# Performance work log

Hardware: AMD Instinct MI355X
Metric: run time of the kernel (lower is better)

## Reference

```python
import jax, jax.numpy as jnp
import numpy as np

EPS = 1e-5

def _conv1x1(x, w, b):
    # x: [B,C,H,W], w: [O,C], b: [O]  (1x1 conv == channel matmul)
    return jnp.einsum('bchw,oc->bohw', x, w) + b[None, :, None, None]

def _bn_relu(y, gamma, beta, mean, var):
    inv = gamma / jnp.sqrt(var + EPS)
    return jax.nn.relu(y * inv[None, :, None, None] + (beta - mean * inv)[None, :, None, None])

def setup_inputs() -> dict:
    key = jax.random.key(0)
    ks = jax.random.split(key, 8)
    B, C, H, W = 8, 2048, 48, 48
    mid = C // 4  # k = 4 -> mid_ch = 512
    s_in = (2.0 / C) ** 0.5   # kaiming-like scale for 1x1 convs from C channels
    s_mid = (2.0 / mid) ** 0.5
    return {
        'x': jax.random.normal(ks[0], (B, C, H, W), jnp.float32),
        'f_w': jax.random.normal(ks[1], (mid, C), jnp.float32) * s_in,
        'f_b': jnp.zeros((mid,), jnp.float32),
        'f_gamma': jnp.ones((mid,), jnp.float32),
        'f_beta': jnp.zeros((mid,), jnp.float32),
        'f_mean': jnp.zeros((mid,), jnp.float32),
        'f_var': jnp.ones((mid,), jnp.float32),
        'g_w': jax.random.normal(ks[2], (mid, C), jnp.float32) * s_in,
        'g_b': jnp.zeros((mid,), jnp.float32),
        'g_gamma': jnp.ones((mid,), jnp.float32),
        'g_beta': jnp.zeros((mid,), jnp.float32),
        'g_mean': jnp.zeros((mid,), jnp.float32),
        'g_var': jnp.ones((mid,), jnp.float32),
        'h_w': jax.random.normal(ks[3], (mid, C), jnp.float32) * s_in,
        'h_b': jnp.zeros((mid,), jnp.float32),
        'v_w': jax.random.normal(ks[4], (C, mid), jnp.float32) * s_mid,
        'v_b': jnp.zeros((C,), jnp.float32),
    }

def reference(x, f_w, f_b, f_gamma, f_beta, f_mean, f_var,
              g_w, g_b, g_gamma, g_beta, g_mean, g_var,
              h_w, h_b, v_w, v_b):
    B, C, H, W = x.shape
    mid = f_w.shape[0]
    N = H * W
    f_x = _bn_relu(_conv1x1(x, f_w, f_b), f_gamma, f_beta, f_mean, f_var).reshape(B, mid, N)
    g_x = _bn_relu(_conv1x1(x, g_w, g_b), g_gamma, g_beta, g_mean, g_var).reshape(B, mid, N)
    h_x = _conv1x1(x, h_w, h_b).reshape(B, mid, N)
    # z = f_x^T @ g_x : [B, N, N]
    scores = jnp.einsum('bcn,bcm->bnm', f_x, g_x) * (mid ** -0.5)
    attn = jax.nn.softmax(scores, axis=-1)
    # z = attn @ h_x^T : [B, N, mid] -> [B, mid, H, W]
    z = jnp.einsum('bnm,bcm->bcn', attn, h_x).reshape(B, mid, H, W)
    z = jnp.einsum('bchw,oc->bohw', z, v_w) + v_b[None, :, None, None]
    return (z + x, attn)
```

## Files before the change

kernel.cpp:

```cpp
#include <hip/hip_runtime.h>
#include <math.h>

typedef unsigned short u16;
typedef unsigned short u16x4 __attribute__((ext_vector_type(4)));
typedef unsigned short u16x8 __attribute__((ext_vector_type(8)));
typedef __bf16 bf16x8 __attribute__((ext_vector_type(8)));
typedef float f32x4 __attribute__((ext_vector_type(4)));

typedef __attribute__((address_space(1))) const unsigned int gu32;
typedef __attribute__((address_space(3))) unsigned int su32;

#define B_ 8
#define C_ 2048
#define MID_ 512
#define N_ 2304

#define BAR() do { asm volatile("" ::: "memory"); __builtin_amdgcn_s_barrier(); asm volatile("" ::: "memory"); } while (0)

#define QMFMA(AV, BV, MO, NO)                                                             \
  { _Pragma("unroll") for (int mfi = 0; mfi < 4; ++mfi) {                                 \
      _Pragma("unroll") for (int nfi = 0; nfi < 2; ++nfi) {                               \
        acc[MO + mfi][NO + nfi] = __builtin_amdgcn_mfma_f32_16x16x32_bf16(                \
            AV[0][mfi], BV[0][nfi], acc[MO + mfi][NO + nfi], 0, 0, 0);                    \
        acc[MO + mfi][NO + nfi] = __builtin_amdgcn_mfma_f32_16x16x32_bf16(                \
            AV[1][mfi], BV[1][nfi], acc[MO + mfi][NO + nfi], 0, 0, 0); } } }

static __device__ __forceinline__ u16 f2bf(float f) {
  union { float f; unsigned u; } c; c.f = f;
  unsigned u = c.u;
  u += 0x7fffu + ((u >> 16) & 1u);
  return (u16)(u >> 16);
}
static __device__ __forceinline__ float bf2f(u16 x) {
  union { unsigned u; float f; } c; c.u = ((unsigned)x) << 16; return c.f;
}

__global__ __launch_bounds__(256) void prep_all_k(
    const float* __restrict__ fw, const float* __restrict__ gw,
    const float* __restrict__ hw, const float* __restrict__ vw,
    const float* fb, const float* fg, const float* fbe, const float* fm, const float* fv,
    const float* gb, const float* gg, const float* gbe, const float* gm, const float* gv,
    const float* hb,
    u16* __restrict__ wall, u16* __restrict__ vwb,
    float* __restrict__ scale, float* __restrict__ bias) {
  const int gid = blockIdx.x * 256 + threadIdx.x;
  if (gid < 393216) {
    int e = gid * 8; int r = e >> 11;
    const float* s = (r < 512) ? (fw + e) : (r < 1024) ? (gw + e - (512 << 11)) : (hw + e - (1024 << 11));
    float4 v0 = *(const float4*)s, v1 = *(const float4*)(s + 4);
    u16x8 w;
    w[0]=f2bf(v0.x); w[1]=f2bf(v0.y); w[2]=f2bf(v0.z); w[3]=f2bf(v0.w);
    w[4]=f2bf(v1.x); w[5]=f2bf(v1.y); w[6]=f2bf(v1.z); w[7]=f2bf(v1.w);
    *(u16x8*)&wall[e] = w;
  } else if (gid < 524288) {
    int e = (gid - 393216) * 8;
    float4 v0 = *(const float4*)(vw + e), v1 = *(const float4*)(vw + e + 4);
    u16x8 w;
    w[0]=f2bf(v0.x); w[1]=f2bf(v0.y); w[2]=f2bf(v0.z); w[3]=f2bf(v0.w);
    w[4]=f2bf(v1.x); w[5]=f2bf(v1.y); w[6]=f2bf(v1.z); w[7]=f2bf(v1.w);
    *(u16x8*)&vwb[e] = w;
  }
  if (gid < 1536) {
    const float FS = 0.044194173824159216f;
    int i = gid;
    if (i < 512) {
      float inv = fg[i] / sqrtf(fv[i] + 1e-5f);
      scale[i] = inv * FS; bias[i] = (fb[i] * inv + fbe[i] - fm[i] * inv) * FS;
    } else if (i < 1024) {
      int j = i - 512;
      float inv = gg[j] / sqrtf(gv[j] + 1e-5f);
      scale[i] = inv; bias[i] = gb[j] * inv + gbe[j] - gm[j] * inv;
    } else {
      scale[i] = 1.0f; bias[i] = hb[i - 1024];
    }
  }
}

__global__ __launch_bounds__(256) void transpose_x_k(const float* __restrict__ x, u16* __restrict__ xT) {
  __shared__ float tile[64][68];
  const int b = blockIdx.z;
  const int n0 = blockIdx.x * 64, c0 = blockIdx.y * 64;
  const float* xb = x + (size_t)b * C_ * N_;
  u16* xTb = xT + (size_t)b * N_ * C_;
  const int r = threadIdx.x >> 2, q = threadIdx.x & 3;
  #pragma unroll
  for (int j = 0; j < 4; ++j) {
    float4 v = *(const float4*)&xb[(size_t)(c0 + r) * N_ + n0 + (q + 4 * j) * 4];
    *(float4*)&tile[r][(q + 4 * j) * 4] = v;
  }
  __syncthreads();
  #pragma unroll
  for (int g = 0; g < 2; ++g) {
    const int cl = (q * 2 + g) * 8;
    u16x8 w;
    #pragma unroll
    for (int e = 0; e < 8; ++e) w[e] = f2bf(tile[cl + e][r]);
    *(u16x8*)&xTb[(size_t)(n0 + r) * C_ + c0 + cl] = w;
  }
}

__global__ __launch_bounds__(256) void transpose_h_k(const u16* __restrict__ fghT, u16* __restrict__ hx) {
  __shared__ u16 tile[64][72];
  const int b = blockIdx.z;
  const int n0 = blockIdx.x * 64, c0 = blockIdx.y * 64;
  const u16* src = fghT + (size_t)b * N_ * 1536;
  u16* dst = hx + (size_t)b * MID_ * N_;
  const int r = threadIdx.x >> 2, q = threadIdx.x & 3;
  #pragma unroll
  for (int g = 0; g < 2; ++g) {
    const int cl = q * 16 + g * 8;
    *(u16x8*)&tile[r][cl] = *(const u16x8*)&src[(size_t)(n0 + r) * 1536 + 1024 + c0 + cl];
  }
  __syncthreads();
  #pragma unroll
  for (int g = 0; g < 2; ++g) {
    const int cl = q * 16 + g * 8;
    u16x8 w;
    #pragma unroll
    for (int e = 0; e < 8; ++e) w[e] = tile[cl + e][r];
    *(u16x8*)&dst[(size_t)(c0 + r) * N_ + n0 + cl] = w;
  }
}

#define EP_FG 0
#define EP_SCALE16 1
#define EP_FINAL 2

template<int EPI, int SWZ, int GX, int GY>
__global__ __launch_bounds__(512, 2) void gemm5_kernel(
    const u16* __restrict__ Ag, int lda, long long sA,
    const u16* __restrict__ Bg, int ldb, long long sB,
    void* __restrict__ Cg, int ldc, long long sC, int K,
    const float* __restrict__ ep_scale, const float* __restrict__ ep_bias,
    const float* __restrict__ ep_x, long long sX)
{
  extern __shared__ __align__(16) u16 smem[];
  u16* As = smem;
  u16* Bs = smem + 2 * 256 * 64;

  int tx, ty, tz;
  {
    const int L = blockIdx.x;
    const int xcd = L & 7, r = L >> 3;
    if constexpr (SWZ == 0) {
      const int i = r % GX, j = (r / GX) * 8 + xcd;
      tx = i; ty = j % GY; tz = j / GY;
    } else if constexpr (SWZ == 1) {
      const int i = r % GY, j = (r / GY) * 8 + xcd;
      ty = i; tx = j % GX; tz = j / GX;
    } else {
      const int i = r % 9, jg = (r / 9) * 8 + xcd;
      const int bx = jg % (GX / 3), rem = jg / (GX / 3);
      const int by = rem % (GY / 3); tz = rem / (GY / 3);
      tx = bx * 3 + i % 3; ty = by * 3 + i / 3;
    }
  }

  const int tid = threadIdx.x;
  const int lane = tid & 63;
  const int wv = tid >> 6;
  const int b = tz;
  const int m0 = ty * 256;
  const int n0 = tx * 256;
  const int wm = (wv >> 2) * 128;
  const int wn = (wv & 3) * 64;
  const int lr = lane & 15, lg = lane >> 4;

  const u16* Ab = Ag + (size_t)b * sA;
  const u16* Bb = Bg + (size_t)b * sB;
  const int nk = K >> 6;

  const int srow = lane >> 3;
  const int sksw = ((lane & 7) ^ srow) * 8;
  const int rdsw0 = ((0 + lg) ^ (lr & 7)) * 8;
  const int rdsw1 = ((4 + lg) ^ (lr & 7)) * 8;

  f32x4 acc[8][4];
  #pragma unroll
  for (int i = 0; i < 8; ++i)
    #pragma unroll
    for (int j = 0; j < 4; ++j)
      acc[i][j] = f32x4{0.f, 0.f, 0.f, 0.f};

  auto STAGE_A = [&](int p2, int t) {
    #pragma unroll
    for (int j = 0; j < 4; ++j) {
      const int rb = j * 64 + wv * 8;
      const u16* g = Ab + (size_t)(m0 + rb + srow) * lda + t * 64 + sksw;
      __builtin_amdgcn_global_load_lds((gu32*)g, (su32*)(As + p2 * 16384 + rb * 64), 16, 0, 0);
    }
  };
  auto STAGE_B = [&](int p2, int t) {
    #pragma unroll
    for (int j = 0; j < 4; ++j) {
      const int rb = j * 64 + wv * 8;
      const u16* g = Bb + (size_t)(n0 + rb + srow) * ldb + t * 64 + sksw;
      __builtin_amdgcn_global_load_lds((gu32*)g, (su32*)(Bs + p2 * 16384 + rb * 64), 16, 0, 0);
    }
  };

  STAGE_A(0, 0); STAGE_B(0, 0);
  if (nk > 1) { STAGE_A(1, 1); STAGE_B(1, 1); }

  for (int kt = 0; kt < nk; ++kt) {
    const int p = kt & 1;
    if (kt + 1 < nk) asm volatile("s_waitcnt vmcnt(8)" ::: "memory");
    else             asm volatile("s_waitcnt vmcnt(0)" ::: "memory");
    BAR();

    const u16* Asl = As + p * 16384;
    const u16* Bsl = Bs + p * 16384;
    const bool st = (kt + 2) < nk;
    const int ps = (kt + 2) & 1;

    bf16x8 aV[2][4], bLo[2][2], bHi[2][2];

    #pragma unroll
    for (int ks = 0; ks < 2; ++ks) {
      const int ro = ks ? rdsw1 : rdsw0;
      #pragma unroll
      for (int i = 0; i < 4; ++i)
        aV[ks][i] = *(const bf16x8*)(Asl + (wm + i * 16 + lr) * 64 + ro);
      #pragma unroll
      for (int i = 0; i < 2; ++i)
        bLo[ks][i] = *(const bf16x8*)(Bsl + (wn + i * 16 + lr) * 64 + ro);
    }
    BAR();
    __builtin_amdgcn_s_setprio(1);
    QMFMA(aV, bLo, 0, 0);
    __builtin_amdgcn_s_setprio(0);
    BAR();

    #pragma unroll
    for (int ks = 0; ks < 2; ++ks) {
      const int ro = ks ? rdsw1 : rdsw0;
      #pragma unroll
      for (int i = 0; i < 2; ++i)
        bHi[ks][i] = *(const bf16x8*)(Bsl + (wn + 32 + i * 16 + lr) * 64 + ro);
    }
    BAR();
    __builtin_amdgcn_s_setprio(1);
    QMFMA(aV, bHi, 0, 2);
    __builtin_amdgcn_s_setprio(0);
    BAR();

    #pragma unroll
    for (int ks = 0; ks < 2; ++ks) {
      const int ro = ks ? rdsw1 : rdsw0;
      #pragma unroll
      for (int i = 0; i < 4; ++i)
        aV[ks][i] = *(const bf16x8*)(Asl + (wm + 64 + i * 16 + lr) * 64 + ro);
    }
    if (st) STAGE_B(ps, kt + 2);
    BAR();
    __builtin_amdgcn_s_setprio(1);
    QMFMA(aV, bLo, 4, 0);
    __builtin_amdgcn_s_setprio(0);
    BAR();

    if (st) STAGE_A(ps, kt + 2);
    BAR();
    __builtin_amdgcn_s_setprio(1);
    QMFMA(aV, bHi, 4, 2);
    __builtin_amdgcn_s_setprio(0);
    BAR();
  }

  u16*   C16 = (u16*)Cg + (size_t)b * sC;
  float* C32 = (float*)Cg + (size_t)b * sC;
  const float* xb = (EPI == EP_FINAL) ? (ep_x + (size_t)b * sX) : nullptr;
  #pragma unroll
  for (int mf = 0; mf < 8; ++mf) {
    #pragma unroll
    for (int nf = 0; nf < 4; ++nf) {
      #pragma unroll
      for (int r = 0; r < 4; ++r) {
        int row = m0 + wm + mf * 16 + lg * 4 + r;
        int col = n0 + wn + nf * 16 + lr;
        float v = acc[mf][nf][r];
        if constexpr (EPI == EP_FG) {
          v = v * ep_scale[col] + ep_bias[col];
          if (col < 1024) v = fmaxf(v, 0.f);
          C16[(size_t)row * ldc + col] = f2bf(v);
        } else if constexpr (EPI == EP_SCALE16) {
          C16[(size_t)row * ldc + col] = f2bf(v);
        } else {
          v += ep_bias[row] + xb[(size_t)row * ldc + col];
          C32[(size_t)row * ldc + col] = v;
        }
      }
    }
  }
}

__global__ __launch_bounds__(256) void softmax_k(u16* __restrict__ SP, float* __restrict__ attn) {
  const int l = threadIdx.x & 63;
  const size_t row = (size_t)blockIdx.x * 4 + (threadIdx.x >> 6);
  u16* sp = SP + row * N_;
  float* ar = attn + row * N_;

  u16x8 s[4];
  #pragma unroll
  for (int j = 0; j < 4; ++j) s[j] = *(const u16x8*)&sp[j * 512 + l * 8];
  u16x4 st4 = *(const u16x4*)&sp[2048 + l * 4];

  float v[4][8], t[4];
  float mx = -3.0e38f;
  #pragma unroll
  for (int j = 0; j < 4; ++j)
    #pragma unroll
    for (int e = 0; e < 8; ++e) { v[j][e] = bf2f(s[j][e]); mx = fmaxf(mx, v[j][e]); }
  #pragma unroll
  for (int e = 0; e < 4; ++e) { t[e] = bf2f(st4[e]); mx = fmaxf(mx, t[e]); }
  #pragma unroll
  for (int o = 32; o; o >>= 1) mx = fmaxf(mx, __shfl_xor(mx, o));

  float sum = 0.f;
  #pragma unroll
  for (int j = 0; j < 4; ++j)
    #pragma unroll
    for (int e = 0; e < 8; ++e) { v[j][e] = __expf(v[j][e] - mx); sum += v[j][e]; }
  #pragma unroll
  for (int e = 0; e < 4; ++e) { t[e] = __expf(t[e] - mx); sum += t[e]; }
  #pragma unroll
  for (int o = 32; o; o >>= 1) sum += __shfl_xor(sum, o);
  const float inv = 1.0f / sum;

  #pragma unroll
  for (int j = 0; j < 4; ++j) {
    float4 lo = {v[j][0] * inv, v[j][1] * inv, v[j][2] * inv, v[j][3] * inv};
    float4 hi = {v[j][4] * inv, v[j][5] * inv, v[j][6] * inv, v[j][7] * inv};
    *(float4*)&ar[j * 512 + l * 8] = lo;
    *(float4*)&ar[j * 512 + l * 8 + 4] = hi;
    u16x8 p8;
    p8[0]=f2bf(lo.x); p8[1]=f2bf(lo.y); p8[2]=f2bf(lo.z); p8[3]=f2bf(lo.w);
    p8[4]=f2bf(hi.x); p8[5]=f2bf(hi.y); p8[6]=f2bf(hi.z); p8[7]=f2bf(hi.w);
    *(u16x8*)&sp[j * 512 + l * 8] = p8;
  }
  float4 tl = {t[0] * inv, t[1] * inv, t[2] * inv, t[3] * inv};
  *(float4*)&ar[2048 + l * 4] = tl;
  u16x4 p4; p4[0]=f2bf(tl.x); p4[1]=f2bf(tl.y); p4[2]=f2bf(tl.z); p4[3]=f2bf(tl.w);
  *(u16x4*)&sp[2048 + l * 4] = p4;
}

extern "C" void kernel_launch(void* const* d_in, const int* in_sizes, int n_in,
                              void* d_out, int out_size, void* d_ws, size_t ws_size,
                              hipStream_t stream) {
  const float* x    = (const float*)d_in[0];
  const float* f_w  = (const float*)d_in[1];
  const float* f_b  = (const float*)d_in[2];
  const float* f_ga = (const float*)d_in[3];
  const float* f_be = (const float*)d_in[4];
  const float* f_me = (const float*)d_in[5];
  const float* f_va = (const float*)d_in[6];
  const float* g_w  = (const float*)d_in[7];
  const float* g_b  = (const float*)d_in[8];
  const float* g_ga = (const float*)d_in[9];
  const float* g_be = (const float*)d_in[10];
  const float* g_me = (const float*)d_in[11];
  const float* g_va = (const float*)d_in[12];
  const float* h_w  = (const float*)d_in[13];
  const float* h_b  = (const float*)d_in[14];
  const float* v_w  = (const float*)d_in[15];
  const float* v_b  = (const float*)d_in[16];

  float* out0 = (float*)d_out;
  float* attn = out0 + (size_t)B_ * C_ * N_;

  char* p = (char*)d_ws;
  u16* xT   = (u16*)p; p += (size_t)B_ * N_ * C_ * 2;
  u16* fghT = (u16*)p; p += (size_t)B_ * N_ * 1536 * 2;
  u16* hx   = (u16*)p; p += (size_t)B_ * MID_ * N_ * 2;
  u16* ZT   = (u16*)p; p += (size_t)B_ * N_ * MID_ * 2;
  u16* Wall = (u16*)p; p += (size_t)1536 * C_ * 2;
  u16* vwb  = (u16*)p; p += (size_t)C_ * MID_ * 2;
  float* sc = (float*)p; p += 1536 * 4;
  float* bi = (float*)p; p += 1536 * 4;
  p = (char*)(((size_t)p + 255) & ~(size_t)255);
  u16* SP   = (u16*)p; p += (size_t)B_ * N_ * N_ * 2;

  hipFuncSetAttribute((const void*)gemm5_kernel<EP_FG, 0, 6, 9>,      hipFuncAttributeMaxDynamicSharedMemorySize, 131072);
  hipFuncSetAttribute((const void*)gemm5_kernel<EP_SCALE16, 2, 9, 9>, hipFuncAttributeMaxDynamicSharedMemorySize, 131072);
  hipFuncSetAttribute((const void*)gemm5_kernel<EP_SCALE16, 0, 2, 9>, hipFuncAttributeMaxDynamicSharedMemorySize, 131072);
  hipFuncSetAttribute((const void*)gemm5_kernel<EP_FINAL, 1, 9, 8>,   hipFuncAttributeMaxDynamicSharedMemorySize, 131072);

  prep_all_k<<<2048, 256, 0, stream>>>(f_w, g_w, h_w, v_w,
                                       f_b, f_ga, f_be, f_me, f_va,
                                       g_b, g_ga, g_be, g_me, g_va, h_b,
                                       Wall, vwb, sc, bi);
  transpose_x_k<<<dim3(N_ / 64, C_ / 64, B_), 256, 0, stream>>>(x, xT);

  gemm5_kernel<EP_FG, 0, 6, 9><<<dim3(6 * 9 * 8), 512, 131072, stream>>>(
      xT, C_, (long long)N_ * C_, Wall, C_, 0,
      fghT, 1536, (long long)N_ * 1536, C_, sc, bi, nullptr, 0);

  transpose_h_k<<<dim3(N_ / 64, MID_ / 64, B_), 256, 0, stream>>>(fghT, hx);

  gemm5_kernel<EP_SCALE16, 2, 9, 9><<<dim3(9 * 9 * 8), 512, 131072, stream>>>(
      fghT, 1536, (long long)N_ * 1536, fghT + 512, 1536, (long long)N_ * 1536,
      SP, N_, (long long)N_ * N_, MID_, nullptr, nullptr, nullptr, 0);

  softmax_k<<<(B_ * N_) / 4, 256, 0, stream>>>(SP, attn);

  gemm5_kernel<EP_SCALE16, 0, 2, 9><<<dim3(2 * 9 * 8), 512, 131072, stream>>>(
      SP, N_, (long long)N_ * N_, hx, N_, (long long)MID_ * N_,
      ZT, MID_, (long long)N_ * MID_, N_, nullptr, nullptr, nullptr, 0);

  gemm5_kernel<EP_FINAL, 1, 9, 8><<<dim3(9 * 8 * 8), 512, 131072, stream>>>(
      vwb, MID_, 0, ZT, MID_, (long long)N_ * MID_,
      out0, N_, (long long)C_ * N_, MID_, nullptr, v_b, x, (long long)C_ * N_);
}
```

Measured before the change: 504.3 us.

## Merge prep/transpose launches and stage bf16 GEMM epilogue through LDS

Merges the weight prep kernel into the x transpose kernel, and the h transpose into the softmax kernel, by splitting each launch's block range. This removes two kernel launches and lets the smaller jobs fill in around the larger ones. The bf16 GEMM epilogues now write each 16-row fragment into a free LDS buffer and read it back as 16-byte row segments, replacing scattered 2-byte global stores. The risk is that the reused LDS buffer could still be live for other waves, and the extra LDS round trip adds latency.

```diff
diff --git a/kernel.cpp b/kernel.cpp
--- a/kernel.cpp
+++ b/kernel.cpp
@@ -35,7 +35,8 @@
   union { unsigned u; float f; } c; c.u = ((unsigned)x) << 16; return c.f;
 }
 
-__global__ __launch_bounds__(256) void prep_all_k(
+__global__ __launch_bounds__(256) void txp_k(
+    const float* __restrict__ x, u16* __restrict__ xT,
     const float* __restrict__ fw, const float* __restrict__ gw,
     const float* __restrict__ hw, const float* __restrict__ vw,
     const float* fb, const float* fg, const float* fbe, const float* fm, const float* fv,
@@ -43,82 +44,59 @@
     const float* hb,
     u16* __restrict__ wall, u16* __restrict__ vwb,
     float* __restrict__ scale, float* __restrict__ bias) {
-  const int gid = blockIdx.x * 256 + threadIdx.x;
-  if (gid < 393216) {
-    int e = gid * 8; int r = e >> 11;
-    const float* s = (r < 512) ? (fw + e) : (r < 1024) ? (gw + e - (512 << 11)) : (hw + e - (1024 << 11));
-    float4 v0 = *(const float4*)s, v1 = *(const float4*)(s + 4);
-    u16x8 w;
-    w[0]=f2bf(v0.x); w[1]=f2bf(v0.y); w[2]=f2bf(v0.z); w[3]=f2bf(v0.w);
-    w[4]=f2bf(v1.x); w[5]=f2bf(v1.y); w[6]=f2bf(v1.z); w[7]=f2bf(v1.w);
-    *(u16x8*)&wall[e] = w;
-  } else if (gid < 524288) {
-    int e = (gid - 393216) * 8;
-    float4 v0 = *(const float4*)(vw + e), v1 = *(const float4*)(vw + e + 4);
-    u16x8 w;
-    w[0]=f2bf(v0.x); w[1]=f2bf(v0.y); w[2]=f2bf(v0.z); w[3]=f2bf(v0.w);
-    w[4]=f2bf(v1.x); w[5]=f2bf(v1.y); w[6]=f2bf(v1.z); w[7]=f2bf(v1.w);
-    *(u16x8*)&vwb[e] = w;
-  }
-  if (gid < 1536) {
-    const float FS = 0.044194173824159216f;
-    int i = gid;
-    if (i < 512) {
-      float inv = fg[i] / sqrtf(fv[i] + 1e-5f);
-      scale[i] = inv * FS; bias[i] = (fb[i] * inv + fbe[i] - fm[i] * inv) * FS;
-    } else if (i < 1024) {
-      int j = i - 512;
-      float inv = gg[j] / sqrtf(gv[j] + 1e-5f);
-      scale[i] = inv; bias[i] = gb[j] * inv + gbe[j] - gm[j] * inv;
-    } else {
-      scale[i] = 1.0f; bias[i] = hb[i - 1024];
-    }
-  }
-}
-
-__global__ __launch_bounds__(256) void transpose_x_k(const float* __restrict__ x, u16* __restrict__ xT) {
   __shared__ float tile[64][68];
-  const int b = blockIdx.z;
-  const int n0 = blockIdx.x * 64, c0 = blockIdx.y * 64;
-  const float* xb = x + (size_t)b * C_ * N_;
-  u16* xTb = xT + (size_t)b * N_ * C_;
-  const int r = threadIdx.x >> 2, q = threadIdx.x & 3;
-  #pragma unroll
-  for (int j = 0; j < 4; ++j) {
-    float4 v = *(const float4*)&xb[(size_t)(c0 + r) * N_ + n0 + (q + 4 * j) * 4];
-    *(float4*)&tile[r][(q + 4 * j) * 4] = v;
-  }
-  __syncthreads();
-  #pragma unroll
-  for (int g = 0; g < 2; ++g) {
-    const int cl = (q * 2 + g) * 8;
-    u16x8 w;
-    #pragma unroll
-    for (int e = 0; e < 8; ++e) w[e] = f2bf(tile[cl + e][r]);
-    *(u16x8*)&xTb[(size_t)(n0 + r) * C_ + c0 + cl] = w;
-  }
-}
-
-__global__ __launch_bounds__(256) void transpose_h_k(const u16* __restrict__ fghT, u16* __restrict__ hx) {
-  __shared__ u16 tile[64][72];
-  const int b = blockIdx.z;
-  const int n0 = blockIdx.x * 64, c0 = blockIdx.y * 64;
-  const u16* src = fghT + (size_t)b * N_ * 1536;
-  u16* dst = hx + (size_t)b * MID_ * N_;
-  const int r = threadIdx.x >> 2, q = threadIdx.x & 3;
-  #pragma unroll
-  for (int g = 0; g < 2; ++g) {
-    const int cl = q * 16 + g * 8;
-    *(u16x8*)&tile[r][cl] = *(const u16x8*)&src[(size_t)(n0 + r) * 1536 + 1024 + c0 + cl];
-  }
-  __syncthreads();
-  #pragma unroll
-  for (int g = 0; g < 2; ++g) {
-    const int cl = q * 16 + g * 8;
-    u16x8 w;
-    #pragma unroll
-    for (int e = 0; e < 8; ++e) w[e] = tile[cl + e][r];
-    *(u16x8*)&dst[(size_t)(c0 + r) * N_ + n0 + cl] = w;
+  const int bid = blockIdx.x;
+  if (bid < 9216) {
+    const int n0 = (bid % 36) * 64, c0 = ((bid / 36) % 32) * 64, b = bid / 1152;
+    const float* xb = x + (size_t)b * C_ * N_;
+    u16* xTb = xT + (size_t)b * N_ * C_;
+    const int r = threadIdx.x >> 2, q = threadIdx.x & 3;
+    #pragma unroll
+    for (int j = 0; j < 4; ++j) {
+      float4 v = *(const float4*)&xb[(size_t)(c0 + r) * N_ + n0 + (q + 4 * j) * 4];
+      *(float4*)&tile[r][(q + 4 * j) * 4] = v;
+    }
+    __syncthreads();
+    #pragma unroll
+    for (int g = 0; g < 2; ++g) {
+      const int cl = (q * 2 + g) * 8;
+      u16x8 w;
+      #pragma unroll
+      for (int e = 0; e < 8; ++e) w[e] = f2bf(tile[cl + e][r]);
+      *(u16x8*)&xTb[(size_t)(n0 + r) * C_ + c0 + cl] = w;
+    }
+  } else {
+    const int gid = (bid - 9216) * 256 + threadIdx.x;
+    if (gid < 393216) {
+      int e = gid * 8; int r = e >> 11;
+      const float* s = (r < 512) ? (fw + e) : (r < 1024) ? (gw + e - (512 << 11)) : (hw + e - (1024 << 11));
+      float4 v0 = *(const float4*)s, v1 = *(const float4*)(s + 4);
+      u16x8 w;
+      w[0]=f2bf(v0.x); w[1]=f2bf(v0.y); w[2]=f2bf(v0.z); w[3]=f2bf(v0.w);
+      w[4]=f2bf(v1.x); w[5]=f2bf(v1.y); w[6]=f2bf(v1.z); w[7]=f2bf(v1.w);
+      *(u16x8*)&wall[e] = w;
+    } else if (gid < 524288) {
+      int e = (gid - 393216) * 8;
+      float4 v0 = *(const float4*)(vw + e), v1 = *(const float4*)(vw + e + 4);
+      u16x8 w;
+      w[0]=f2bf(v0.x); w[1]=f2bf(v0.y); w[2]=f2bf(v0.z); w[3]=f2bf(v0.w);
+      w[4]=f2bf(v1.x); w[5]=f2bf(v1.y); w[6]=f2bf(v1.z); w[7]=f2bf(v1.w);
+      *(u16x8*)&vwb[e] = w;
+    }
+    if (gid < 1536) {
+      const float FS = 0.044194173824159216f;
+      int i = gid;
+      if (i < 512) {
+        float inv = fg[i] / sqrtf(fv[i] + 1e-5f);
+        scale[i] = inv * FS; bias[i] = (fb[i] * inv + fbe[i] - fm[i] * inv) * FS;
+      } else if (i < 1024) {
+        int j = i - 512;
+        float inv = gg[j] / sqrtf(gv[j] + 1e-5f);
+        scale[i] = inv; bias[i] = gb[j] * inv + gbe[j] - gm[j] * inv;
+      } else {
+        scale[i] = 1.0f; bias[i] = hb[i - 1024];
+      }
+    }
   }
 }
 
@@ -268,79 +246,122 @@
 
   u16*   C16 = (u16*)Cg + (size_t)b * sC;
   float* C32 = (float*)Cg + (size_t)b * sC;
-  const float* xb = (EPI == EP_FINAL) ? (ep_x + (size_t)b * sX) : nullptr;
-  #pragma unroll
-  for (int mf = 0; mf < 8; ++mf) {
-    #pragma unroll
-    for (int nf = 0; nf < 4; ++nf) {
-      #pragma unroll
-      for (int r = 0; r < 4; ++r) {
-        int row = m0 + wm + mf * 16 + lg * 4 + r;
-        int col = n0 + wn + nf * 16 + lr;
-        float v = acc[mf][nf][r];
-        if constexpr (EPI == EP_FG) {
-          v = v * ep_scale[col] + ep_bias[col];
-          if (col < 1024) v = fmaxf(v, 0.f);
-          C16[(size_t)row * ldc + col] = f2bf(v);
-        } else if constexpr (EPI == EP_SCALE16) {
-          C16[(size_t)row * ldc + col] = f2bf(v);
-        } else {
-          v += ep_bias[row] + xb[(size_t)row * ldc + col];
+  if constexpr (EPI == EP_FINAL) {
+    const float* xb = ep_x + (size_t)b * sX;
+    #pragma unroll
+    for (int mf = 0; mf < 8; ++mf) {
+      #pragma unroll
+      for (int nf = 0; nf < 4; ++nf) {
+        #pragma unroll
+        for (int r = 0; r < 4; ++r) {
+          int row = m0 + wm + mf * 16 + lg * 4 + r;
+          int col = n0 + wn + nf * 16 + lr;
+          float v = acc[mf][nf][r] + ep_bias[row] + xb[(size_t)row * ldc + col];
           C32[(size_t)row * ldc + col] = v;
         }
       }
     }
+  } else {
+    const int plo = ((nk - 1) & 1) ^ 1;
+    u16* scr = As + plo * 16384 + wv * 2048;
+    const int r_ = lane & 15, seg = lane >> 4;
+    #pragma unroll
+    for (int mf = 0; mf < 8; ++mf) {
+      u16* h = scr + (mf & 1) * 1024;
+      #pragma unroll
+      for (int nf = 0; nf < 4; ++nf) {
+        #pragma unroll
+        for (int r = 0; r < 4; ++r) {
+          int col = n0 + wn + nf * 16 + lr;
+          float v = acc[mf][nf][r];
+          if constexpr (EPI == EP_FG) {
+            v = v * ep_scale[col] + ep_bias[col];
+            if (col < 1024) v = fmaxf(v, 0.f);
+          }
+          h[(lg * 4 + r) * 64 + nf * 16 + lr] = f2bf(v);
+        }
+      }
+      asm volatile("s_waitcnt lgkmcnt(0)" ::: "memory");
+      __builtin_amdgcn_sched_barrier(0);
+      u16x8 w0 = *(const u16x8*)(h + r_ * 64 + seg * 16);
+      u16x8 w1 = *(const u16x8*)(h + r_ * 64 + seg * 16 + 8);
+      u16* dst = C16 + (size_t)(m0 + wm + mf * 16 + r_) * ldc + (n0 + wn + seg * 16);
+      *(u16x8*)dst = w0;
+      *(u16x8*)(dst + 8) = w1;
+    }
   }
 }
 
-__global__ __launch_bounds__(256) void softmax_k(u16* __restrict__ SP, float* __restrict__ attn) {
-  const int l = threadIdx.x & 63;
-  const size_t row = (size_t)blockIdx.x * 4 + (threadIdx.x >> 6);
-  u16* sp = SP + row * N_;
-  float* ar = attn + row * N_;
-
-  u16x8 s[4];
-  #pragma unroll
-  for (int j = 0; j < 4; ++j) s[j] = *(const u16x8*)&sp[j * 512 + l * 8];
-  u16x4 st4 = *(const u16x4*)&sp[2048 + l * 4];
-
-  float v[4][8], t[4];
-  float mx = -3.0e38f;
-  #pragma unroll
-  for (int j = 0; j < 4; ++j)
-    #pragma unroll
-    for (int e = 0; e < 8; ++e) { v[j][e] = bf2f(s[j][e]); mx = fmaxf(mx, v[j][e]); }
-  #pragma unroll
-  for (int e = 0; e < 4; ++e) { t[e] = bf2f(st4[e]); mx = fmaxf(mx, t[e]); }
-  #pragma unroll
-  for (int o = 32; o; o >>= 1) mx = fmaxf(mx, __shfl_xor(mx, o));
-
-  float sum = 0.f;
-  #pragma unroll
-  for (int j = 0; j < 4; ++j)
-    #pragma unroll
-    for (int e = 0; e < 8; ++e) { v[j][e] = __expf(v[j][e] - mx); sum += v[j][e]; }
-  #pragma unroll
-  for (int e = 0; e < 4; ++e) { t[e] = __expf(t[e] - mx); sum += t[e]; }
-  #pragma unroll
-  for (int o = 32; o; o >>= 1) sum += __shfl_xor(sum, o);
-  const float inv = 1.0f / sum;
-
-  #pragma unroll
-  for (int j = 0; j < 4; ++j) {
-    float4 lo = {v[j][0] * inv, v[j][1] * inv, v[j][2] * inv, v[j][3] * inv};
-    float4 hi = {v[j][4] * inv, v[j][5] * inv, v[j][6] * inv, v[j][7] * inv};
-    *(float4*)&ar[j * 512 + l * 8] = lo;
-    *(float4*)&ar[j * 512 + l * 8 + 4] = hi;
-    u16x8 p8;
-    p8[0]=f2bf(lo.x); p8[1]=f2bf(lo.y); p8[2]=f2bf(lo.z); p8[3]=f2bf(lo.w);
-    p8[4]=f2bf(hi.x); p8[5]=f2bf(hi.y); p8[6]=f2bf(hi.z); p8[7]=f2bf(hi.w);
-    *(u16x8*)&sp[j * 512 + l * 8] = p8;
+__global__ __launch_bounds__(256) void softmax_th_k(
+    u16* __restrict__ SP, float* __restrict__ attn,
+    const u16* __restrict__ fghT, u16* __restrict__ hx) {
+  __shared__ u16 tile[64][72];
+  const int bid = blockIdx.x;
+  if (bid < 4608) {
+    const int l = threadIdx.x & 63;
+    const size_t row = (size_t)bid * 4 + (threadIdx.x >> 6);
+    u16* sp = SP + row * N_;
+    float* ar = attn + row * N_;
+    u16x8 s[4];
+    #pragma unroll
+    for (int j = 0; j < 4; ++j) s[j] = *(const u16x8*)&sp[j * 512 + l * 8];
+    u16x4 st4 = *(const u16x4*)&sp[2048 + l * 4];
+    float v[4][8], t[4];
+    float mx = -3.0e38f;
+    #pragma unroll
+    for (int j = 0; j < 4; ++j)
+      #pragma unroll
+      for (int e = 0; e < 8; ++e) { v[j][e] = bf2f(s[j][e]); mx = fmaxf(mx, v[j][e]); }
+    #pragma unroll
+    for (int e = 0; e < 4; ++e) { t[e] = bf2f(st4[e]); mx = fmaxf(mx, t[e]); }
+    #pragma unroll
+    for (int o = 32; o; o >>= 1) mx = fmaxf(mx, __shfl_xor(mx, o));
+    float sum = 0.f;
+    #pragma unroll
+    for (int j = 0; j < 4; ++j)
+      #pragma unroll
+      for (int e = 0; e < 8; ++e) { v[j][e] = __expf(v[j][e] - mx); sum += v[j][e]; }
+    #pragma unroll
+    for (int e = 0; e < 4; ++e) { t[e] = __expf(t[e] - mx); sum += t[e]; }
+    #pragma unroll
+    for (int o = 32; o; o >>= 1) sum += __shfl_xor(sum, o);
+    const float inv = 1.0f / sum;
+    #pragma unroll
+    for (int j = 0; j < 4; ++j) {
+      float4 lo = {v[j][0] * inv, v[j][1] * inv, v[j][2] * inv, v[j][3] * inv};
+      float4 hi = {v[j][4] * inv, v[j][5] * inv, v[j][6] * inv, v[j][7] * inv};
+      *(float4*)&ar[j * 512 + l * 8] = lo;
+      *(float4*)&ar[j * 512 + l * 8 + 4] = hi;
+      u16x8 p8;
+      p8[0]=f2bf(lo.x); p8[1]=f2bf(lo.y); p8[2]=f2bf(lo.z); p8[3]=f2bf(lo.w);
+      p8[4]=f2bf(hi.x); p8[5]=f2bf(hi.y); p8[6]=f2bf(hi.z); p8[7]=f2bf(hi.w);
+      *(u16x8*)&sp[j * 512 + l * 8] = p8;
+    }
+    float4 tl = {t[0] * inv, t[1] * inv, t[2] * inv, t[3] * inv};
+    *(float4*)&ar[2048 + l * 4] = tl;
+    u16x4 p4; p4[0]=f2bf(tl.x); p4[1]=f2bf(tl.y); p4[2]=f2bf(tl.z); p4[3]=f2bf(tl.w);
+    *(u16x4*)&sp[2048 + l * 4] = p4;
+  } else {
+    const int t = bid - 4608;
+    const int n0 = (t % 36) * 64, c0 = ((t / 36) % 8) * 64, b = t / 288;
+    const u16* src = fghT + (size_t)b * N_ * 1536;
+    u16* dst = hx + (size_t)b * MID_ * N_;
+    const int r = threadIdx.x >> 2, q = threadIdx.x & 3;
+    #pragma unroll
+    for (int g = 0; g < 2; ++g) {
+      const int cl = q * 16 + g * 8;
+      *(u16x8*)&tile[r][cl] = *(const u16x8*)&src[(size_t)(n0 + r) * 1536 + 1024 + c0 + cl];
+    }
+    __syncthreads();
+    #pragma unroll
+    for (int g = 0; g < 2; ++g) {
+      const int cl = q * 16 + g * 8;
+      u16x8 w;
+      #pragma unroll
+      for (int e = 0; e < 8; ++e) w[e] = tile[cl + e][r];
+      *(u16x8*)&dst[(size_t)(c0 + r) * N_ + n0 + cl] = w;
+    }
   }
-  float4 tl = {t[0] * inv, t[1] * inv, t[2] * inv, t[3] * inv};
-  *(float4*)&ar[2048 + l * 4] = tl;
-  u16x4 p4; p4[0]=f2bf(tl.x); p4[1]=f2bf(tl.y); p4[2]=f2bf(tl.z); p4[3]=f2bf(tl.w);
-  *(u16x4*)&sp[2048 + l * 4] = p4;
 }
 
 extern "C" void kernel_launch(void* const* d_in, const int* in_sizes, int n_in,
@@ -384,23 +405,20 @@
   hipFuncSetAttribute((const void*)gemm5_kernel<EP_SCALE16, 0, 2, 9>, hipFuncAttributeMaxDynamicSharedMemorySize, 131072);
   hipFuncSetAttribute((const void*)gemm5_kernel<EP_FINAL, 1, 9, 8>,   hipFuncAttributeMaxDynamicSharedMemorySize, 131072);
 
-  prep_all_k<<<2048, 256, 0, stream>>>(f_w, g_w, h_w, v_w,
-                                       f_b, f_ga, f_be, f_me, f_va,
-                                       g_b, g_ga, g_be, g_me, g_va, h_b,
-                                       Wall, vwb, sc, bi);
-  transpose_x_k<<<dim3(N_ / 64, C_ / 64, B_), 256, 0, stream>>>(x, xT);
+  txp_k<<<11264, 256, 0, stream>>>(x, xT, f_w, g_w, h_w, v_w,
+                                   f_b, f_ga, f_be, f_me, f_va,
+                                   g_b, g_ga, g_be, g_me, g_va, h_b,
+                                   Wall, vwb, sc, bi);
 
   gemm5_kernel<EP_FG, 0, 6, 9><<<dim3(6 * 9 * 8), 512, 131072, stream>>>(
       xT, C_, (long long)N_ * C_, Wall, C_, 0,
       fghT, 1536, (long long)N_ * 1536, C_, sc, bi, nullptr, 0);
 
-  transpose_h_k<<<dim3(N_ / 64, MID_ / 64, B_), 256, 0, stream>>>(fghT, hx);
-
   gemm5_kernel<EP_SCALE16, 2, 9, 9><<<dim3(9 * 9 * 8), 512, 131072, stream>>>(
       fghT, 1536, (long long)N_ * 1536, fghT + 512, 1536, (long long)N_ * 1536,
       SP, N_, (long long)N_ * N_, MID_, nullptr, nullptr, nullptr, 0);
 
-  softmax_k<<<(B_ * N_) / 4, 256, 0, stream>>>(SP, attn);
+  softmax_th_k<<<6912, 256, 0, stream>>>(SP, attn, fghT, hx);
 
   gemm5_kernel<EP_SCALE16, 0, 2, 9><<<dim3(2 * 9 * 8), 512, 131072, stream>>>(
       SP, N_, (long long)N_ * N_, hx, N_, (long long)MID_ * N_,
```

Result: faster. 489.2 us (-3.0%).
